# Kernel optimization log

Hardware: AMD Instinct MI355X
Metric: run time of the kernel (lower is better)

The kernel has to match this reference:

```python
import jax, jax.numpy as jnp
import numpy as np

NUM_CAPS = 8
NITER = 3
TAU = 1.0
N_NODES = 50000
N_EDGES = 800000
D_FEAT = 128


def _l2norm(v):
    # matches torch fn.normalize(dim=-1, eps=1e-12): v / max(||v||, eps)
    n = jnp.linalg.norm(v, axis=-1, keepdims=True)
    return v / jnp.maximum(n, 1e-12)


def setup_inputs() -> dict:
    key = jax.random.key(0)
    k1, k2, k3 = jax.random.split(key, 3)
    x = jax.random.normal(k1, (N_NODES, D_FEAT), dtype=jnp.float32)
    src = jax.random.randint(k2, (N_EDGES,), 0, N_NODES)
    trg = jax.random.randint(k3, (N_EDGES,), 0, N_NODES)
    edge_index = jnp.stack([src, trg], axis=0).astype(jnp.int64)
    return {"x": x, "edge_index": edge_index}


def reference(x, edge_index):
    num_node, num_dim = x.shape
    dpc = num_dim // NUM_CAPS  # dim per capsule
    src, trg = edge_index[0], edge_index[1]

    xc = _l2norm(x.reshape(num_node, NUM_CAPS, dpc))  # [N, C, d]
    z = xc[src]                                        # [E, C, d] gathered source caps
    u = xc
    for _ in range(NITER):
        # per-edge, per-capsule agreement score
        p = jnp.einsum('ecd,ecd->ec', z, u[trg])       # [E, C]
        p = jax.nn.softmax(p / TAU, axis=1)
        msg = z * p[:, :, None]                        # [E, C, d]
        u = jax.ops.segment_sum(msg, trg, num_segments=num_node)  # [N, C, d]
        u = _l2norm(u + xc)
    return u.reshape(num_node, num_dim)
```

## Files before the change

### kernel.cpp

```cpp
#include <hip/hip_runtime.h>
#include <hip/hip_bf16.h>

#define DF   128
#define DPC  16
#define KCAP 62
#define RWRD 32

#define NB_ROUTE 2048
#define NB_PREP  2048
#define NB_ZERO  257

__device__ __forceinline__ float cap_sum(float v) {
    v += __shfl_xor(v, 1);
    v += __shfl_xor(v, 2);
    v += __shfl_xor(v, 4);
    return v;
}
__device__ __forceinline__ float bits_lo(unsigned int w) {
    union { unsigned int u; float f; } c; c.u = w << 16; return c.f;
}
__device__ __forceinline__ float bits_hi(unsigned int w) {
    union { unsigned int u; float f; } c; c.u = w & 0xFFFF0000u; return c.f;
}
__device__ __forceinline__ unsigned int f2b_pack(float lo, float hi) {
    __hip_bfloat16 a = __float2bfloat16(lo), b = __float2bfloat16(hi);
    unsigned short ua = *reinterpret_cast<unsigned short*>(&a);
    unsigned short ub = *reinterpret_cast<unsigned short*>(&b);
    return ((unsigned int)ub << 16) | ua;
}
__device__ __forceinline__ float2 load_x2(const void* __restrict__ xraw, int fp32,
                                          int node, int lane) {
    size_t off = (size_t)node * DF + (size_t)lane * 2;
    if (fp32) {
        return *reinterpret_cast<const float2*>((const float*)xraw + off);
    } else {
        unsigned int w = ((const unsigned int*)xraw)[(size_t)node * 64 + lane];
        return make_float2(bits_lo(w), bits_hi(w));
    }
}
__device__ __forceinline__ int2 edge_st(const int* __restrict__ ei, int i64,
                                        int e, int n_edges) {
    size_t si = i64 ? (size_t)2 * e             : (size_t)e;
    size_t ti = i64 ? (size_t)2 * (n_edges + e) : (size_t)(n_edges + e);
    return make_int2(ei[si], ei[ti]);
}
__device__ __forceinline__ void proc_pk(const uint4& w0, const uint4& w1,
                                        bool valid, const float* u, float* acc) {
    unsigned ww[8] = {w0.x, w0.y, w0.z, w0.w, w1.x, w1.y, w1.z, w1.w};
    float p = 0.0f;
    #pragma unroll
    for (int q = 0; q < 8; ++q) {
        p = fmaf(bits_lo(ww[q]), u[2*q],   p);
        p = fmaf(bits_hi(ww[q]), u[2*q+1], p);
    }
    float ex = __expf(p);
    float sd = ex;
    sd += __shfl_xor(sd, 1);
    sd += __shfl_xor(sd, 2);
    sd += __shfl_xor(sd, 4);
    float w = valid ? ex * __builtin_amdgcn_rcpf(sd) : 0.0f;
    #pragma unroll
    for (int q = 0; q < 8; ++q) {
        acc[2*q]   = fmaf(w, bits_lo(ww[q]), acc[2*q]);
        acc[2*q+1] = fmaf(w, bits_hi(ww[q]), acc[2*q+1]);
    }
}

__global__ void k_detect_zero(const unsigned int* __restrict__ xw,
                              const unsigned int* __restrict__ ew,
                              int* __restrict__ flags, int* __restrict__ bkt,
                              int n_nodes) {
    if (blockIdx.x == 0) {
        __shared__ int s_nan, s_zero;
        int tid = threadIdx.x;
        if (tid == 0) { s_nan = 0; s_zero = 0; }
        __syncthreads();
        int cnt_nan = 0;
        for (int i = tid; i < 4096; i += 256) {
            unsigned int lo = xw[i] & 0xFFFFu;
            if ((lo & 0x7F80u) == 0x7F80u) cnt_nan++;
        }
        int cnt_zero = 0;
        for (int i = tid; i < 1024; i += 256) {
            if (ew[2 * i + 1] == 0u) cnt_zero++;
        }
        atomicAdd(&s_nan, cnt_nan);
        atomicAdd(&s_zero, cnt_zero);
        __syncthreads();
        if (tid == 0) {
            flags[0] = (s_nan > 0) ? 1 : 0;
            flags[1] = (s_zero > 512) ? 1 : 0;
        }
    } else {
        int total = n_nodes * (RWRD / 4);
        int stride = (NB_ZERO - 1) * 256;
        for (int i = (blockIdx.x - 1) * 256 + threadIdx.x; i < total; i += stride)
            reinterpret_cast<uint4*>(bkt)[i] = make_uint4(0u, 0u, 0u, 0u);
    }
}

__global__ void k_prep(const void* __restrict__ xraw, unsigned int* __restrict__ xcb,
                       const int* __restrict__ ei, int* __restrict__ bkt,
                       const int* __restrict__ flags,
                       int n_nodes, int n_edges) {
    const int fp32 = flags[0];
    const int lane = threadIdx.x & 63;
    const int gw   = (blockIdx.x * blockDim.x + threadIdx.x) >> 6;
    const int nw   = (gridDim.x * blockDim.x) >> 6;

    for (int wid = gw; wid < n_nodes; wid += nw) {
        float2 v = load_x2(xraw, fp32, wid, lane);
        float ss = cap_sum(v.x * v.x + v.y * v.y);
        float scale = 1.0f / fmaxf(sqrtf(ss), 1e-12f);
        int c = lane >> 3, jp = lane & 7;
        int w = (jp < 4) ? (c * 4 + jp) : (32 + c * 4 + (jp - 4));
        xcb[(size_t)wid * 64 + w] = f2b_pack(v.x * scale, v.y * scale);
    }

    const int i64 = flags[1];
    const int gtid = blockIdx.x * blockDim.x + threadIdx.x;
    const int gth  = gridDim.x * blockDim.x;
    for (int e = gtid; e < n_edges; e += gth) {
        int2 st = edge_st(ei, i64, e, n_edges);
        if ((unsigned)st.x < (unsigned)n_nodes &&
            (unsigned)st.y < (unsigned)n_nodes) {
            unsigned* row = (unsigned*)(bkt + (size_t)st.y * RWRD);
            int slot = atomicAdd((int*)row, 1);
            if (slot < KCAP) {
                int us   = 2 + slot;
                unsigned val = (unsigned)(unsigned short)st.x << (16 * (us & 1));
                atomicOr(row + (us >> 1), val);
            }
        }
    }
}

__global__ void __launch_bounds__(256)
k_route(const int* __restrict__ bkt,
        const unsigned int* __restrict__ xcb,
        float* __restrict__ u_out, int n_nodes) {
    const int lane = threadIdx.x & 63;
    const int gw   = (blockIdx.x * blockDim.x + threadIdx.x) >> 6;
    const int nw   = (gridDim.x * blockDim.x) >> 6;
    const int e8 = lane >> 3;
    const int c  = lane & 7;
    const int coff = c * 16;
    const char* __restrict__ xb = (const char*)xcb;

    for (int t = gw; t < n_nodes; t += nw) {
        unsigned rw = ((const unsigned*)(bkt + (size_t)t * RWRD))[lane & 31];

        size_t trow = (size_t)t << 8;
        uint4 t0 = *reinterpret_cast<const uint4*>(xb + trow + coff);
        uint4 t1 = *reinterpret_cast<const uint4*>(xb + trow + 128 + coff);

        int deg = __builtin_amdgcn_readfirstlane((int)rw);
        deg = min(deg, KCAP);

        auto nid = [&](int s) -> int {
            int g = 4 + 2 * s;
            unsigned wv = __shfl(rw, (lane & 32) | (g >> 2));
            return (int)((g & 2) ? (wv >> 16) : (wv & 0xFFFFu));
        };

        int off0 = 0, off1 = 0, off2 = 0;
        {
            int s0 = e8,      c0 = (s0 < deg) ? s0 : 0;
            int s1 = e8 + 8,  c1 = (s1 < deg) ? s1 : 0;
            int s2 = e8 + 16, c2 = (s2 < deg) ? s2 : 0;
            if (deg > 0)  off0 = nid(c0) << 8;
            if (deg > 8)  off1 = nid(c1) << 8;
            if (deg > 16) off2 = nid(c2) << 8;
        }

        unsigned tw[8] = {t0.x, t0.y, t0.z, t0.w, t1.x, t1.y, t1.z, t1.w};
        float ss = 0.0f;
        #pragma unroll
        for (int q = 0; q < 8; ++q) {
            float xl = bits_lo(tw[q]), xh = bits_hi(tw[q]);
            ss = fmaf(xl, xl, ss);
            ss = fmaf(xh, xh, ss);
        }
        float sc = __builtin_amdgcn_rsqf(fmaxf(ss, 1e-24f));
        float u[DPC];
        #pragma unroll
        for (int q = 0; q < 8; ++q) {
            u[2*q]   = bits_lo(tw[q]) * sc;
            u[2*q+1] = bits_hi(tw[q]) * sc;
        }

        for (int it = 0; it < 3; ++it) {
            asm volatile("" ::: "memory");

            uint4 a0, b0, a1, b1, a2, b2;
            if (deg > 0) {
                a0 = *reinterpret_cast<const uint4*>(xb + off0 + coff);
                b0 = *reinterpret_cast<const uint4*>(xb + off0 + 128 + coff);
            }
            if (deg > 8) {
                a1 = *reinterpret_cast<const uint4*>(xb + off1 + coff);
                b1 = *reinterpret_cast<const uint4*>(xb + off1 + 128 + coff);
            }
            float acc[DPC];
            #pragma unroll
            for (int j = 0; j < DPC; ++j) acc[j] = 0.0f;

            if (deg > 0)  proc_pk(a0, b0, e8 < deg, u, acc);
            if (deg > 16) {
                a2 = *reinterpret_cast<const uint4*>(xb + off2 + coff);
                b2 = *reinterpret_cast<const uint4*>(xb + off2 + 128 + coff);
            }
            if (deg > 8)  proc_pk(a1, b1, 8  + e8 < deg, u, acc);
            if (deg > 16) proc_pk(a2, b2, 16 + e8 < deg, u, acc);
            if (deg > 24) {
                for (int base = 24; base < deg; base += 8) {
                    int s  = base + e8;
                    int sl = (s < deg) ? s : 0;
                    int off = nid(sl) << 8;
                    uint4 a = *reinterpret_cast<const uint4*>(xb + off + coff);
                    uint4 b = *reinterpret_cast<const uint4*>(xb + off + 128 + coff);
                    proc_pk(a, b, s < deg, u, acc);
                }
            }

            #pragma unroll
            for (int j = 0; j < DPC; ++j) {
                acc[j] += __shfl_xor(acc[j], 8);
                acc[j] += __shfl_xor(acc[j], 16);
                acc[j] += __shfl_xor(acc[j], 32);
            }
            float s2 = 0.0f;
            #pragma unroll
            for (int q = 0; q < 8; ++q) {
                float xl = bits_lo(tw[q]) * sc;
                float xh = bits_hi(tw[q]) * sc;
                u[2*q]   = acc[2*q]   + xl;
                u[2*q+1] = acc[2*q+1] + xh;
                s2 = fmaf(u[2*q],   u[2*q],   s2);
                s2 = fmaf(u[2*q+1], u[2*q+1], s2);
            }
            float sc2 = __builtin_amdgcn_rsqf(fmaxf(s2, 1e-24f));
            #pragma unroll
            for (int j = 0; j < DPC; ++j) u[j] *= sc2;
        }

        if (e8 == 0) {
            float* dst = u_out + (size_t)t * DF + c * DPC;
            #pragma unroll
            for (int j = 0; j < DPC; j += 4)
                *reinterpret_cast<float4*>(dst + j) =
                    make_float4(u[j], u[j+1], u[j+2], u[j+3]);
        }
    }
}

extern "C" void kernel_launch(void* const* d_in, const int* in_sizes, int n_in,
                              void* d_out, int out_size, void* d_ws, size_t ws_size,
                              hipStream_t stream) {
    const void* x  = d_in[0];
    const int*  ei = (const int*)d_in[1];
    const int n_nodes = in_sizes[0] / DF;
    const int n_edges = in_sizes[1] / 2;
    const size_t NC = (size_t)n_nodes * DF;

    unsigned int* xcb = (unsigned int*)d_ws;
    int* bkt   = (int*)(xcb + NC / 2);
    int* flags = bkt + (size_t)n_nodes * RWRD;

    float* u_out = (float*)d_out;

    k_detect_zero<<<NB_ZERO, 256, 0, stream>>>(
        (const unsigned int*)x, (const unsigned int*)ei, flags, bkt, n_nodes);
    k_prep<<<NB_PREP, 256, 0, stream>>>(x, xcb, ei, bkt, flags,
                                        n_nodes, n_edges);
    k_route<<<NB_ROUTE, 256, 0, stream>>>(bkt, xcb, u_out, n_nodes);
}
```

Baseline: 280.9 us.

## Stage neighbor rows in LDS via async global_load_lds and split bucket layout

Moves per-node degree counters into a separate strided array, which spreads atomics across cache lines, and stores neighbor ids as plain u16 writes instead of atomicOr. The first 24 neighbor feature rows are prefetched once into per-wave LDS with global_load_lds and reused across all three routing iterations, rather than re-read from global memory each iteration. Prep is split into separate normalize and bucket kernels, and grid sizes plus a waves-per-eu hint are changed. The cost is more LDS per block (24 KB), which may limit occupancy, plus an extra kernel launch.

```diff
diff --git a/kernel.cpp b/kernel.cpp
--- a/kernel.cpp
+++ b/kernel.cpp
@@ -3,12 +3,12 @@
 
 #define DF   128
 #define DPC  16
-#define KCAP 62
-#define RWRD 32
-
-#define NB_ROUTE 2048
-#define NB_PREP  2048
-#define NB_ZERO  257
+#define KCAP 64
+
+#define NB_XC    2048
+#define NB_BKT   2048
+#define NB_ROUTE 1536
+#define NB_ZERO  64
 
 __device__ __forceinline__ float cap_sum(float v) {
     v += __shfl_xor(v, 1);
@@ -37,12 +37,6 @@
         unsigned int w = ((const unsigned int*)xraw)[(size_t)node * 64 + lane];
         return make_float2(bits_lo(w), bits_hi(w));
     }
-}
-__device__ __forceinline__ int2 edge_st(const int* __restrict__ ei, int i64,
-                                        int e, int n_edges) {
-    size_t si = i64 ? (size_t)2 * e             : (size_t)e;
-    size_t ti = i64 ? (size_t)2 * (n_edges + e) : (size_t)(n_edges + e);
-    return make_int2(ei[si], ei[ti]);
 }
 __device__ __forceinline__ void proc_pk(const uint4& w0, const uint4& w1,
                                         bool valid, const float* u, float* acc) {
@@ -68,8 +62,8 @@
 
 __global__ void k_detect_zero(const unsigned int* __restrict__ xw,
                               const unsigned int* __restrict__ ew,
-                              int* __restrict__ flags, int* __restrict__ bkt,
-                              int n_nodes) {
+                              int* __restrict__ flags, int* __restrict__ cnt,
+                              int zwords) {
     if (blockIdx.x == 0) {
         __shared__ int s_nan, s_zero;
         int tid = threadIdx.x;
@@ -92,85 +86,103 @@
             flags[1] = (s_zero > 512) ? 1 : 0;
         }
     } else {
-        int total = n_nodes * (RWRD / 4);
         int stride = (NB_ZERO - 1) * 256;
-        for (int i = (blockIdx.x - 1) * 256 + threadIdx.x; i < total; i += stride)
-            reinterpret_cast<uint4*>(bkt)[i] = make_uint4(0u, 0u, 0u, 0u);
-    }
-}
-
-__global__ void k_prep(const void* __restrict__ xraw, unsigned int* __restrict__ xcb,
-                       const int* __restrict__ ei, int* __restrict__ bkt,
-                       const int* __restrict__ flags,
-                       int n_nodes, int n_edges) {
+        for (int i = (blockIdx.x - 1) * 256 + threadIdx.x; i < zwords; i += stride)
+            cnt[i] = 0;
+    }
+}
+
+__global__ void k_xc(const void* __restrict__ xraw,
+                     unsigned int* __restrict__ xcb,
+                     const int* __restrict__ flags, int n_nodes) {
     const int fp32 = flags[0];
     const int lane = threadIdx.x & 63;
     const int gw   = (blockIdx.x * blockDim.x + threadIdx.x) >> 6;
     const int nw   = (gridDim.x * blockDim.x) >> 6;
-
     for (int wid = gw; wid < n_nodes; wid += nw) {
         float2 v = load_x2(xraw, fp32, wid, lane);
         float ss = cap_sum(v.x * v.x + v.y * v.y);
         float scale = 1.0f / fmaxf(sqrtf(ss), 1e-12f);
-        int c = lane >> 3, jp = lane & 7;
-        int w = (jp < 4) ? (c * 4 + jp) : (32 + c * 4 + (jp - 4));
+        int cc = lane >> 3, jp = lane & 7;
+        int w = (jp < 4) ? (cc * 4 + jp) : (32 + cc * 4 + (jp - 4));
         xcb[(size_t)wid * 64 + w] = f2b_pack(v.x * scale, v.y * scale);
     }
-
+}
+
+__global__ void k_bucket(const int* __restrict__ ei,
+                         int* __restrict__ cnt, int cstr,
+                         unsigned short* __restrict__ rows,
+                         const int* __restrict__ flags,
+                         int n_nodes, int n_edges) {
     const int i64 = flags[1];
     const int gtid = blockIdx.x * blockDim.x + threadIdx.x;
     const int gth  = gridDim.x * blockDim.x;
     for (int e = gtid; e < n_edges; e += gth) {
-        int2 st = edge_st(ei, i64, e, n_edges);
-        if ((unsigned)st.x < (unsigned)n_nodes &&
-            (unsigned)st.y < (unsigned)n_nodes) {
-            unsigned* row = (unsigned*)(bkt + (size_t)st.y * RWRD);
-            int slot = atomicAdd((int*)row, 1);
-            if (slot < KCAP) {
-                int us   = 2 + slot;
-                unsigned val = (unsigned)(unsigned short)st.x << (16 * (us & 1));
-                atomicOr(row + (us >> 1), val);
-            }
+        int s, t;
+        if (i64) {
+            long sv = ((const long*)ei)[e];
+            long tv = ((const long*)ei)[(size_t)n_edges + e];
+            s = (int)sv; t = (int)tv;
+        } else {
+            s = ei[e]; t = ei[(size_t)n_edges + e];
+        }
+        if ((unsigned)s < (unsigned)n_nodes && (unsigned)t < (unsigned)n_nodes) {
+            int slot = atomicAdd(cnt + (size_t)t * cstr, 1);
+            if (slot < KCAP)
+                rows[(size_t)t * KCAP + slot] = (unsigned short)s;
         }
     }
 }
 
 __global__ void __launch_bounds__(256)
-k_route(const int* __restrict__ bkt,
+__attribute__((amdgpu_waves_per_eu(8)))
+k_route(const unsigned short* __restrict__ rows,
         const unsigned int* __restrict__ xcb,
+        const int* __restrict__ cnt, int cstr,
         float* __restrict__ u_out, int n_nodes) {
+    __shared__ char smem[4 * 6144];
     const int lane = threadIdx.x & 63;
-    const int gw   = (blockIdx.x * blockDim.x + threadIdx.x) >> 6;
-    const int nw   = (gridDim.x * blockDim.x) >> 6;
+    char* wbase = smem + (threadIdx.x >> 6) * 6144;
+    const int gw = (blockIdx.x * blockDim.x + threadIdx.x) >> 6;
+    const int nw = (gridDim.x * blockDim.x) >> 6;
     const int e8 = lane >> 3;
     const int c  = lane & 7;
     const int coff = c * 16;
     const char* __restrict__ xb = (const char*)xcb;
 
     for (int t = gw; t < n_nodes; t += nw) {
-        unsigned rw = ((const unsigned*)(bkt + (size_t)t * RWRD))[lane & 31];
+        const unsigned* wrow = (const unsigned*)(rows + (size_t)t * KCAP);
+        unsigned rw = wrow[lane & 31];
+        int deg = cnt[(size_t)t * cstr];
+        deg = __builtin_amdgcn_readfirstlane(deg);
+        deg = min(deg, KCAP);
 
         size_t trow = (size_t)t << 8;
         uint4 t0 = *reinterpret_cast<const uint4*>(xb + trow + coff);
         uint4 t1 = *reinterpret_cast<const uint4*>(xb + trow + 128 + coff);
 
-        int deg = __builtin_amdgcn_readfirstlane((int)rw);
-        deg = min(deg, KCAP);
-
         auto nid = [&](int s) -> int {
-            int g = 4 + 2 * s;
-            unsigned wv = __shfl(rw, (lane & 32) | (g >> 2));
-            return (int)((g & 2) ? (wv >> 16) : (wv & 0xFFFFu));
+            unsigned wv = __shfl(rw, (lane & 32) | (s >> 1));
+            return (int)((s & 1) ? (wv >> 16) : (wv & 0xFFFFu));
         };
 
-        int off0 = 0, off1 = 0, off2 = 0;
-        {
-            int s0 = e8,      c0 = (s0 < deg) ? s0 : 0;
-            int s1 = e8 + 8,  c1 = (s1 < deg) ? s1 : 0;
-            int s2 = e8 + 16, c2 = (s2 < deg) ? s2 : 0;
-            if (deg > 0)  off0 = nid(c0) << 8;
-            if (deg > 8)  off1 = nid(c1) << 8;
-            if (deg > 16) off2 = nid(c2) << 8;
+        if (deg > 0) {
+            int kmax = (min(deg, 24) + 7) >> 3;
+            for (int k = 0; k < kmax; ++k) {
+                int s  = e8 + 8 * k;
+                int sl = (s < deg) ? s : 0;
+                int off = nid(sl) << 8;
+                const char* ga = xb + off + coff;
+                const char* gb = ga + 128;
+                __builtin_amdgcn_global_load_lds(
+                    (const __attribute__((address_space(1))) unsigned int*)ga,
+                    (__attribute__((address_space(3))) unsigned int*)
+                        (wbase + k * 2048 + (lane << 4)), 16, 0, 0);
+                __builtin_amdgcn_global_load_lds(
+                    (const __attribute__((address_space(1))) unsigned int*)gb,
+                    (__attribute__((address_space(3))) unsigned int*)
+                        (wbase + k * 2048 + 1024 + (lane << 4)), 16, 0, 0);
+            }
         }
 
         unsigned tw[8] = {t0.x, t0.y, t0.z, t0.w, t1.x, t1.y, t1.z, t1.w};
@@ -189,29 +201,25 @@
             u[2*q+1] = bits_hi(tw[q]) * sc;
         }
 
+        asm volatile("s_waitcnt vmcnt(0)" ::: "memory");
+
         for (int it = 0; it < 3; ++it) {
             asm volatile("" ::: "memory");
 
-            uint4 a0, b0, a1, b1, a2, b2;
-            if (deg > 0) {
-                a0 = *reinterpret_cast<const uint4*>(xb + off0 + coff);
-                b0 = *reinterpret_cast<const uint4*>(xb + off0 + 128 + coff);
-            }
-            if (deg > 8) {
-                a1 = *reinterpret_cast<const uint4*>(xb + off1 + coff);
-                b1 = *reinterpret_cast<const uint4*>(xb + off1 + 128 + coff);
-            }
             float acc[DPC];
             #pragma unroll
             for (int j = 0; j < DPC; ++j) acc[j] = 0.0f;
 
-            if (deg > 0)  proc_pk(a0, b0, e8 < deg, u, acc);
-            if (deg > 16) {
-                a2 = *reinterpret_cast<const uint4*>(xb + off2 + coff);
-                b2 = *reinterpret_cast<const uint4*>(xb + off2 + 128 + coff);
-            }
-            if (deg > 8)  proc_pk(a1, b1, 8  + e8 < deg, u, acc);
-            if (deg > 16) proc_pk(a2, b2, 16 + e8 < deg, u, acc);
+            #pragma unroll
+            for (int k = 0; k < 3; ++k) {
+                if (deg > 8 * k) {
+                    uint4 a = *reinterpret_cast<const uint4*>(
+                        wbase + k * 2048 + (lane << 4));
+                    uint4 b = *reinterpret_cast<const uint4*>(
+                        wbase + k * 2048 + 1024 + (lane << 4));
+                    proc_pk(a, b, 8 * k + e8 < deg, u, acc);
+                }
+            }
             if (deg > 24) {
                 for (int base = 24; base < deg; base += 8) {
                     int s  = base + e8;
@@ -263,15 +271,23 @@
     const int n_edges = in_sizes[1] / 2;
     const size_t NC = (size_t)n_nodes * DF;
 
-    unsigned int* xcb = (unsigned int*)d_ws;
-    int* bkt   = (int*)(xcb + NC / 2);
-    int* flags = bkt + (size_t)n_nodes * RWRD;
+    unsigned char* p = (unsigned char*)d_ws;
+    unsigned int*   xcb  = (unsigned int*)p;   p += NC * 2;
+    unsigned short* rows = (unsigned short*)p; p += (size_t)n_nodes * KCAP * 2;
+    int*            flags = (int*)p;           p += 128;
+    int*            cnt  = (int*)p;
+    size_t used  = (size_t)(p - (unsigned char*)d_ws);
+    size_t avail = (ws_size > used) ? (ws_size - used) : 0;
+    int cstr = 32;
+    while (cstr > 1 && (size_t)n_nodes * cstr * sizeof(int) > avail) cstr >>= 1;
+    int zwords = n_nodes * cstr;
 
     float* u_out = (float*)d_out;
 
     k_detect_zero<<<NB_ZERO, 256, 0, stream>>>(
-        (const unsigned int*)x, (const unsigned int*)ei, flags, bkt, n_nodes);
-    k_prep<<<NB_PREP, 256, 0, stream>>>(x, xcb, ei, bkt, flags,
-                                        n_nodes, n_edges);
-    k_route<<<NB_ROUTE, 256, 0, stream>>>(bkt, xcb, u_out, n_nodes);
-}
+        (const unsigned int*)x, (const unsigned int*)ei, flags, cnt, zwords);
+    k_bucket<<<NB_BKT, 256, 0, stream>>>(ei, cnt, cstr, rows, flags,
+                                         n_nodes, n_edges);
+    k_xc<<<NB_XC, 256, 0, stream>>>(x, xcb, flags, n_nodes);
+    k_route<<<NB_ROUTE, 256, 0, stream>>>(rows, xcb, cnt, cstr, u_out, n_nodes);
+}
```

After: 262.7 us. 6.5% less time.
